# Kernel optimization log

Measured on AMD Instinct MI355X. Metric: run time of the kernel, lower is better.

Reference implementation:

```python
import jax, jax.numpy as jnp
import numpy as np

N = 50000      # num nodes
E = 300000     # num edges
C = 256        # channels
H = 8          # num_heads
DH = C // H    # head_dim = 32
NUM_DST = 256  # dst indices live in [0, NUM_DST) -> anchor columns of BFS frontier
MAX_SPD = 3
EPS = 1e-5     # LayerNorm eps (torch default)


def setup_inputs() -> dict:
    key = jax.random.key(0)
    ks = jax.random.split(key, 10)
    scale = 1.0 / np.sqrt(C).astype(np.float32)
    x = jax.random.normal(ks[0], (N, C), jnp.float32)
    src = jax.random.randint(ks[1], (E,), 0, N, dtype=jnp.int32)
    dst = jax.random.randint(ks[2], (E,), 0, NUM_DST, dtype=jnp.int32)
    Wq = jax.random.normal(ks[3], (C, C), jnp.float32) * scale
    Wk = jax.random.normal(ks[4], (C, C), jnp.float32) * scale
    Wv = jax.random.normal(ks[5], (C, C), jnp.float32) * scale
    bq = jax.random.normal(ks[6], (C,), jnp.float32) * scale
    bk = jax.random.normal(ks[7], (C,), jnp.float32) * scale
    bv = jax.random.normal(ks[8], (C,), jnp.float32) * scale
    spd_w = jax.random.normal(ks[9], (MAX_SPD + 2, H), jnp.float32)
    gamma = jnp.ones((C,), jnp.float32)
    beta = jnp.zeros((C,), jnp.float32)
    return dict(x=x, src=src, dst=dst, Wq=Wq, bq=bq, Wk=Wk, bk=bk,
                Wv=Wv, bv=bv, spd_w=spd_w, gamma=gamma, beta=beta)


def _spd_buckets(src, dst):
    # Reverse-BFS shortest-path buckets (use_reverse=True, directed):
    # A[row=dst, col=src]; F_k = bin(A @ F_{k-1}); anchors are dst nodes,
    # which all live in [0, NUM_DST) so the anchor->column map is identity.
    row, col = dst, src
    F = (jnp.arange(N)[:, None] == jnp.arange(NUM_DST)[None, :]).astype(jnp.float32)  # [N, M]
    spd = jnp.full((E,), MAX_SPD + 1, jnp.int32)
    unset = jnp.ones((E,), bool)
    for k in range(1, MAX_SPD + 1):
        # (A @ F)[i] = sum over edges with row==i of F[col]
        F = (jax.ops.segment_sum(F[col], row, num_segments=N) > 0).astype(jnp.float32)
        reach = F[src, dst] > 0
        newly = unset & reach
        spd = jnp.where(newly, k, spd)
        unset = unset & ~newly
    return spd


def _segment_softmax(scores, seg, n):
    # numerically stable softmax over edges grouped by destination node
    m = jax.ops.segment_max(scores, seg, num_segments=n)
    ex = jnp.exp(scores - m[seg])
    s = jax.ops.segment_sum(ex, seg, num_segments=n)
    return ex / s[seg]


def reference(x, src, dst, Wq, bq, Wk, bk, Wv, bv, spd_w, gamma, beta):
    Q = (x @ Wq.T + bq).reshape(N, H, DH)
    K = (x @ Wk.T + bk).reshape(N, H, DH)
    V = (x @ Wv.T + bv).reshape(N, H, DH)
    # per-edge dot-product scores [E, H]
    scores = (Q[dst] * K[src]).sum(-1) / np.float32(np.sqrt(DH))
    spd = jax.lax.stop_gradient(_spd_buckets(src, dst))  # torch.no_grad
    scores = scores + spd_w[spd]
    w = _segment_softmax(scores, dst, N)  # [E, H] (dropout is identity in eval)
    msg = (V[src] * w[:, :, None]).reshape(E, C)
    out = jax.ops.segment_sum(msg, dst, num_segments=N)  # scatter-add aggregation
    # total degree (in + out) broadcast over channels
    ones_e = jnp.ones((E,), jnp.float32)
    deg = jax.ops.segment_sum(ones_e, src, num_segments=N) + \
          jax.ops.segment_sum(ones_e, dst, num_segments=N)
    h = out + deg[:, None] + x  # residual
    mu = h.mean(-1, keepdims=True)
    var = ((h - mu) ** 2).mean(-1, keepdims=True)
    return (h - mu) / jnp.sqrt(var + EPS) * gamma + beta
```

## Files before the change

### kernel.cpp

```cpp
#include <hip/hip_runtime.h>
#include <stdint.h>

#define N_NODES 50000
#define E_EDGES 300000
#define C_CH    256
#define H_HEADS 8
#define NB2     64
#define CHUNK2  4688
#define NBIN    4096
#define SRCDIV  3125
#define NWG_GEMM 1568
#define NWG_LN   12436
#define GOFF     2

typedef unsigned short u16;
typedef unsigned int   u32;

typedef __attribute__((ext_vector_type(8))) short  v8s;
typedef __attribute__((ext_vector_type(4))) float  v4f;

__device__ __forceinline__ float bf2f(u16 v) {
    union { u32 u; float f; } x; x.u = ((u32)v) << 16; return x.f;
}
__device__ __forceinline__ u16 f2bf(float f) {
    union { float f; u32 u; } x; x.f = f;
    u32 r = (x.u + 0x7FFFu + ((x.u >> 16) & 1u)) >> 16;
    return (u16)r;
}
__device__ __forceinline__ void unp2(u32 v, float& lo, float& hi) {
    union { u32 u; float f; } x;
    x.u = v << 16; lo = x.f;
    x.u = v & 0xFFFF0000u; hi = x.f;
}
__device__ __forceinline__ void gl_lds16(const u16* g, u16* l) {
    __builtin_amdgcn_global_load_lds(
        (const __attribute__((address_space(1))) void*)g,
        (__attribute__((address_space(3))) void*)l, 16, 0, 0);
}
__device__ __forceinline__ void pack8(const float4 p, const float4 q, u16* dst) {
    u16 tmp[8];
    tmp[0]=f2bf(p.x); tmp[1]=f2bf(p.y); tmp[2]=f2bf(p.z); tmp[3]=f2bf(p.w);
    tmp[4]=f2bf(q.x); tmp[5]=f2bf(q.y); tmp[6]=f2bf(q.z); tmp[7]=f2bf(q.w);
    *(uint4*)dst = *(const uint4*)tmp;
}

__global__ __launch_bounds__(256) void prep_k(
    const float* __restrict__ Wk, const float* __restrict__ Wv,
    const float* __restrict__ Wq, u16* __restrict__ Wb,
    const int* __restrict__ src, const int* __restrict__ dst,
    u32* __restrict__ blockhist, u32* __restrict__ pinmask,
    u32* __restrict__ zero0)
{
    __shared__ u32 hist[NBIN];
    __shared__ u32 mask[256][8];
    int t = threadIdx.x, b = blockIdx.x;
    if (b < 192) {
        int m = (b < 64) ? 0 : (b < 128) ? 1 : 2;
        const float* sp = (m == 0) ? Wk : (m == 1) ? Wv : Wq;
        u16* dp = Wb + m * 65536;
        int i = (b & 63) * 1024 + t * 4;
        float4 v = *(const float4*)(sp + i);
        ushort4 o;
        o.x = f2bf(v.x); o.y = f2bf(v.y); o.z = f2bf(v.z); o.w = f2bf(v.w);
        *(ushort4*)(dp + i) = o;
        return;
    }
    if (b >= 256) {
        int z = b - 256;
        uint4 zv = make_uint4(0, 0, 0, 0);
        *(uint4*)(zero0 + z * 1024 + t * 4) = zv;
        return;
    }
    int hb = b - 192;
#pragma unroll
    for (int j = 0; j < 16; j++) hist[t + j * 256] = 0;
#pragma unroll
    for (int w = 0; w < 8; w++) mask[t][w] = 0;
    __syncthreads();
    int start = hb * CHUNK2;
    int end = start + CHUNK2; if (end > E_EDGES) end = E_EDGES;
    for (int e = start + t; e < end; e += 256) {
        int d = dst[e], s = src[e];
        atomicAdd(&hist[d * 16 + s / SRCDIV], 1u);
        if (s < 256) atomicOr(&mask[d][s >> 5], 1u << (s & 31));
    }
    __syncthreads();
#pragma unroll
    for (int j = 0; j < 16; j++)
        blockhist[hb * NBIN + t + j * 256] = hist[t + j * 256];
#pragma unroll
    for (int w = 0; w < 8; w++)
        pinmask[hb * 2048 + w * 256 + t] = mask[t][w];
}

__global__ __launch_bounds__(256, 4) void gemm3(
    const float* __restrict__ x, const u16* __restrict__ Wb,
    const float* __restrict__ bk, const float* __restrict__ bv,
    const float* __restrict__ bq,
    u16* __restrict__ Kb, u16* __restrict__ Vb, u16* __restrict__ Qb,
    const u32* __restrict__ blockhist, u32* __restrict__ bin_off,
    const u32* __restrict__ pinmask, unsigned char* __restrict__ T,
    const float* __restrict__ gamma, const float* __restrict__ beta,
    float* __restrict__ y)
{
    __shared__ u16 smem[4][128 * 32];
    const int t = threadIdx.x;

    if (blockIdx.x == 0) {
        u32* tots = (u32*)&smem[0][0];
        u32* tsum = tots + NBIN;
        u32 c[16];
#pragma unroll
        for (int j = 0; j < 16; j++) c[j] = 0;
        for (int b2 = 0; b2 < NB2; b2++) {
#pragma unroll
            for (int j = 0; j < 16; j++)
                c[j] += blockhist[b2 * NBIN + j * 256 + t];
        }
#pragma unroll
        for (int j = 0; j < 16; j++) tots[j * 256 + t] = c[j];
        __syncthreads();
        u32 loc[16]; u32 a = 0;
#pragma unroll
        for (int j = 0; j < 16; j++) { loc[j] = tots[t * 16 + j]; a += loc[j]; }
        tsum[t] = a;
        __syncthreads();
        for (int off = 1; off < 256; off <<= 1) {
            u32 add = (t >= off) ? tsum[t - off] : 0u;
            __syncthreads();
            tsum[t] += add;
            __syncthreads();
        }
        u32 base = tsum[t] - a;
#pragma unroll
        for (int j = 0; j < 16; j++) { bin_off[t * 16 + j] = base; base += loc[j]; }
        if (t == 255) bin_off[NBIN] = base;
        return;
    }
    if (blockIdx.x == 1) {
        u32* b32 = (u32*)&smem[0][0];
        u32 (*F1)[8] = (u32(*)[8])(b32);
        u32 (*F2)[8] = (u32(*)[8])(b32 + 2048);
        u32 (*F3)[8] = (u32(*)[8])(b32 + 4096);
        int i = t;
        u32 mm[8];
#pragma unroll
        for (int w = 0; w < 8; w++) mm[w] = 0;
        for (int b2 = 0; b2 < NB2; b2++) {
#pragma unroll
            for (int w = 0; w < 8; w++)
                mm[w] |= pinmask[b2 * 2048 + w * 256 + i];
        }
#pragma unroll
        for (int w = 0; w < 8; w++) { F1[i][w] = mm[w]; F2[i][w] = 0; F3[i][w] = 0; }
        __syncthreads();
        for (int w = 0; w < 8; w++) {
            u32 m = F1[i][w];
            while (m) {
                int b = __ffs(m) - 1; m &= m - 1;
                int s = w * 32 + b;
#pragma unroll
                for (int j = 0; j < 8; j++) F2[i][j] |= F1[s][j];
            }
        }
        __syncthreads();
        for (int w = 0; w < 8; w++) {
            u32 m = F1[i][w];
            while (m) {
                int b = __ffs(m) - 1; m &= m - 1;
                int s = w * 32 + b;
#pragma unroll
                for (int j = 0; j < 8; j++) F3[i][j] |= F2[s][j];
            }
        }
        __syncthreads();
        for (int w = 0; w < 8; w++) {
            u32 f1 = F1[i][w], f2 = F2[i][w], f3 = F3[i][w];
#pragma unroll
            for (int g = 0; g < 8; g++) {
                u32 word = 0;
#pragma unroll
                for (int b = 0; b < 4; b++) {
                    int bit = g * 4 + b;
                    u32 k = ((f1 >> bit) & 1u) ? 1u : ((f2 >> bit) & 1u) ? 2u
                           : ((f3 >> bit) & 1u) ? 3u : 4u;
                    word |= k << (8 * b);
                }
                *(u32*)(T + i * 256 + w * 32 + g * 4) = word;
            }
        }
        return;
    }
    if (blockIdx.x >= GOFF + NWG_GEMM) {
        int n = (blockIdx.x - (GOFF + NWG_GEMM)) * 4 + (t >> 6) + 256;
        int lane = t & 63;
        int ch = lane * 4;
        float4 xv = *(const float4*)(x + (size_t)n * 256 + ch);
        float h0 = xv.x, h1 = xv.y, h2 = xv.z, h3 = xv.w;
        float s = h0 + h1 + h2 + h3;
#pragma unroll
        for (int off = 1; off < 64; off <<= 1) s += __shfl_xor(s, off);
        float mu = s * (1.0f / 256.0f);
        float d0 = h0 - mu, d1 = h1 - mu, d2 = h2 - mu, d3 = h3 - mu;
        float qq = d0 * d0 + d1 * d1 + d2 * d2 + d3 * d3;
#pragma unroll
        for (int off = 1; off < 64; off <<= 1) qq += __shfl_xor(qq, off);
        float rstd = rsqrtf(qq * (1.0f / 256.0f) + 1e-5f);
        float4 gv = *(const float4*)(gamma + ch);
        float4 bv = *(const float4*)(beta + ch);
        float4 o;
        o.x = d0 * rstd * gv.x + bv.x;
        o.y = d1 * rstd * gv.y + bv.y;
        o.z = d2 * rstd * gv.z + bv.z;
        o.w = d3 * rstd * gv.w + bv.w;
        *(float4*)(y + (size_t)n * 256 + ch) = o;
        return;
    }

    int gid = blockIdx.x - GOFF;
    int xcd = gid & 7, pos = gid >> 3;
    int wgid = xcd * (NWG_GEMM >> 3) + pos;
    int mt, mat, nh;
    if (wgid < 1564) { mt = wgid >> 2; int j = wgid & 3; mat = j >> 1; nh = j & 1; }
    else             { int qi = wgid - 1564; mt = qi >> 1; mat = 2; nh = qi & 1; }
    const int m0 = mt * 128;
    const int M = (mat == 2) ? 256 : N_NODES;
    const u16* W = Wb + mat * 65536;
    const float* bias = (mat == 0) ? bk : (mat == 1) ? bv : bq;
    u16* OUT = (mat == 0) ? Kb : (mat == 1) ? Vb : Qb;
    const int n0 = nh * 128;

    const int lane = t & 63, w = t >> 6;
    const int quad = lane >> 4, l15 = lane & 15;
    const int mq = w & 1, nq = w >> 1;

    v4f acc[16];
#pragma unroll
    for (int i = 0; i < 16; i++) acc[i] = (v4f)(0.0f);

    const int lrow = lane >> 2;
    const int cg   = (lane & 3) * 8;
    int rA0 = m0 + w * 32 + lrow; if (rA0 > 49999) rA0 = 49999;
    int rA1 = rA0 + 16;           if (rA1 > 49999) rA1 = 49999;
    const float* gA0 = x + (size_t)rA0 * 256 + cg;
    const float* gA1 = x + (size_t)rA1 * 256 + cg;
    const u16* gB = W + (size_t)(n0 + w * 32 + lrow) * 256 + (lane & 3) * 8;

    u16* ldsA = &smem[0][(w * 32 + lrow) * 32 + (lane & 3) * 8];

    float4 a00, a01, a10, a11;
#define LOADA(kt) do {                                   \
    a00 = *(const float4*)(gA0 + (kt) * 32);             \
    a01 = *(const float4*)(gA0 + (kt) * 32 + 4);         \
    a10 = *(const float4*)(gA1 + (kt) * 32);             \
    a11 = *(const float4*)(gA1 + (kt) * 32 + 4);         \
} while (0)
#define WRITEA(bi) do {                                  \
    pack8(a00, a01, ldsA + (bi) * 4096);                 \
    pack8(a10, a11, ldsA + (bi) * 4096 + 16 * 32);       \
} while (0)
#define STAGEB(bi, koff) do {                                             \
    gl_lds16(gB + (koff),            &smem[2 + (bi)][(w * 32) * 32]);     \
    gl_lds16(gB + 16 * 256 + (koff), &smem[2 + (bi)][(w * 32 + 16) * 32]);\
} while (0)

    LOADA(0);
    STAGEB(0, 0);
    WRITEA(0);
    __syncthreads();
    for (int kt = 0; kt < 8; kt++) {
        const int cur = kt & 1;
        if (kt < 7) { LOADA(kt + 1); STAGEB(cur ^ 1, (kt + 1) * 32); }
        v8s a[4], b[4];
#pragma unroll
        for (int f = 0; f < 4; f++)
            a[f] = *(const v8s*)(&smem[cur][(mq * 64 + f * 16 + l15) * 32 + quad * 8]);
#pragma unroll
        for (int f = 0; f < 4; f++)
            b[f] = *(const v8s*)(&smem[2 + cur][(nq * 64 + f * 16 + l15) * 32 + quad * 8]);
#pragma unroll
        for (int fm = 0; fm < 4; fm++)
#pragma unroll
            for (int fn = 0; fn < 4; fn++)
                acc[fm * 4 + fn] = __builtin_amdgcn_mfma_f32_16x16x32_bf16(
                    a[fm], b[fn], acc[fm * 4 + fn], 0, 0, 0);
        if (kt < 7) WRITEA(cur ^ 1);
        __syncthreads();
    }
#undef LOADA
#undef WRITEA
#undef STAGEB

    u16* S = &smem[0][0];
#pragma unroll
    for (int fn = 0; fn < 4; fn++) {
        int n = nq * 64 + fn * 16 + l15;
        float bi = bias[n0 + n];
#pragma unroll
        for (int fm = 0; fm < 4; fm++) {
#pragma unroll
            for (int r2 = 0; r2 < 4; r2++) {
                int row = mq * 64 + fm * 16 + quad * 4 + r2;
                S[row * 128 + n] = f2bf(acc[fm * 4 + fn][r2] + bi);
            }
        }
    }
    __syncthreads();
#pragma unroll
    for (int i = 0; i < 8; i++) {
        int c = i * 256 + t;
        int row = c >> 4;
        int m = m0 + row;
        if (m < M)
            *(uint4*)(OUT + (size_t)m * 256 + n0 + (c & 15) * 8) =
                *(const uint4*)(S + c * 8);
    }
}

__global__ __launch_bounds__(256) void base_k(
    const u32* __restrict__ blockhist, const u32* __restrict__ bin_off,
    u32* __restrict__ blockbase)
{
    int bin = blockIdx.x * 256 + threadIdx.x;
    u32 h[NB2];
#pragma unroll
    for (int b = 0; b < NB2; b++) h[b] = blockhist[b * NBIN + bin];
    u32 run = bin_off[bin];
#pragma unroll
    for (int b = 0; b < NB2; b++) {
        blockbase[b * NBIN + bin] = run;
        run += h[b];
    }
}

__global__ __launch_bounds__(256) void scatter2_k(
    const int* __restrict__ src, const int* __restrict__ dst,
    const u32* __restrict__ blockbase, u32* __restrict__ ssrc)
{
    __shared__ u32 cur[NBIN];
    int t = threadIdx.x, b = blockIdx.x;
#pragma unroll
    for (int j = 0; j < 16; j++)
        cur[t + j * 256] = blockbase[b * NBIN + t + j * 256];
    __syncthreads();
    int start = b * CHUNK2;
    int end = start + CHUNK2; if (end > E_EDGES) end = E_EDGES;
    for (int e = start + t; e < end; e += 256) {
        int s = src[e];
        int bin = dst[e] * 16 + s / SRCDIV;
        u32 pos = atomicAdd(&cur[bin], 1u);
        ssrc[pos] = (u32)s;
    }
}

__global__ __launch_bounds__(256) void agg_k(
    const u32* __restrict__ ssrc, const u32* __restrict__ bin_off,
    const u16* __restrict__ Qb, const u16* __restrict__ Kb,
    const u16* __restrict__ Vb, const unsigned char* __restrict__ T,
    const float* __restrict__ spd_w, float* __restrict__ out,
    float* __restrict__ denom)
{
    __shared__ float red[4 * 256];
    __shared__ float dred[4 * 8];
    int bid = blockIdx.x;
    int d = bid >> 4;
    int t = threadIdx.x, lane = t & 63, wave = t >> 6;
    int half = lane >> 5, sl = lane & 31;
    int h = sl >> 2;
    u32 start = bin_off[bid], end = bin_off[bid + 1];

    uint4 qv = *(const uint4*)(Qb + (size_t)d * 256 + sl * 8);
    float q0,q1,q2,q3,q4,q5,q6,q7;
    unp2(qv.x,q0,q1); unp2(qv.y,q2,q3); unp2(qv.z,q4,q5); unp2(qv.w,q6,q7);
    float sw4 = spd_w[4 * 8 + h];

    float a0=0.f,a1=0.f,a2=0.f,a3=0.f,a4=0.f,a5=0.f,a6=0.f,a7=0.f,dsum=0.f;

    u32 i = start + (u32)(wave * 2 + half);
    int s_c = 0, s_n = 0;
    uint4 kv_c = make_uint4(0,0,0,0), vv_c = kv_c;
    if (i < end) {
        s_c = (int)ssrc[i];
        kv_c = *(const uint4*)(Kb + (size_t)s_c * 256 + sl * 8);
        vv_c = *(const uint4*)(Vb + (size_t)s_c * 256 + sl * 8);
        if (i + 8 < end) s_n = (int)ssrc[i + 8];
    }
    while (i < end) {
        u32 inx = i + 8;
        uint4 kv_n = kv_c, vv_n = vv_c;
        if (inx < end) {
            kv_n = *(const uint4*)(Kb + (size_t)s_n * 256 + sl * 8);
            vv_n = *(const uint4*)(Vb + (size_t)s_n * 256 + sl * 8);
        }
        int s_nn = (inx + 8 < end) ? (int)ssrc[inx + 8] : 0;
        float k0,k1,k2,k3,k4,k5,k6,k7, v0,v1,v2,v3,v4,v5,v6,v7;
        unp2(kv_c.x,k0,k1); unp2(kv_c.y,k2,k3); unp2(kv_c.z,k4,k5); unp2(kv_c.w,k6,k7);
        unp2(vv_c.x,v0,v1); unp2(vv_c.y,v2,v3); unp2(vv_c.z,v4,v5); unp2(vv_c.w,v6,v7);
        float p = q0*k0+q1*k1+q2*k2+q3*k3+q4*k4+q5*k5+q6*k6+q7*k7;
        p += __shfl_xor(p, 1);
        p += __shfl_xor(p, 2);
        float bias = (s_c < 256) ? spd_w[(int)T[s_c * 256 + d] * 8 + h] : sw4;
        float wgt = __expf(p * 0.17677669529663689f + bias);
        a0 += wgt*v0; a1 += wgt*v1; a2 += wgt*v2; a3 += wgt*v3;
        a4 += wgt*v4; a5 += wgt*v5; a6 += wgt*v6; a7 += wgt*v7;
        if ((sl & 3) == 0) dsum += wgt;
        i = inx; s_c = s_n; s_n = s_nn; kv_c = kv_n; vv_c = vv_n;
    }
    a0 += __shfl_xor(a0,32); a1 += __shfl_xor(a1,32);
    a2 += __shfl_xor(a2,32); a3 += __shfl_xor(a3,32);
    a4 += __shfl_xor(a4,32); a5 += __shfl_xor(a5,32);
    a6 += __shfl_xor(a6,32); a7 += __shfl_xor(a7,32);
    dsum += __shfl_xor(dsum,32);
    if (half == 0) {
        *(float4*)(&red[wave * 256 + sl * 8])     = make_float4(a0,a1,a2,a3);
        *(float4*)(&red[wave * 256 + sl * 8 + 4]) = make_float4(a4,a5,a6,a7);
        if ((sl & 3) == 0) dred[wave * 8 + h] = dsum;
    }
    __syncthreads();
    float sAll = red[t] + red[256 + t] + red[512 + t] + red[768 + t];
    atomicAdd(&out[(size_t)d * 256 + t], sAll);
    if (t < 8) {
        float ds = dred[t] + dred[8 + t] + dred[16 + t] + dred[24 + t];
        atomicAdd(&denom[d * 8 + t], ds);
    }
}

__global__ __launch_bounds__(256) void ln_k(
    const float* __restrict__ x, const float* __restrict__ out,
    const float* __restrict__ denom, const float* __restrict__ gamma,
    const float* __restrict__ beta, float* __restrict__ y)
{
    int n = blockIdx.x * 4 + (threadIdx.x >> 6);
    int lane = threadIdx.x & 63;
    int ch = lane * 4;
    float4 xv = *(const float4*)(x + (size_t)n * 256 + ch);
    float h0 = xv.x, h1 = xv.y, h2 = xv.z, h3 = xv.w;
    float den = denom[n * 8 + (lane >> 3)];
    float inv = (den > 0.f) ? 1.0f / den : 0.0f;
    const float* op = out + (size_t)n * 256 + ch;
    h0 += op[0] * inv; h1 += op[1] * inv;
    h2 += op[2] * inv; h3 += op[3] * inv;
    float s = h0 + h1 + h2 + h3;
#pragma unroll
    for (int off = 1; off < 64; off <<= 1) s += __shfl_xor(s, off);
    float mu = s * (1.0f / 256.0f);
    float d0 = h0 - mu, d1 = h1 - mu, d2 = h2 - mu, d3 = h3 - mu;
    float q = d0 * d0 + d1 * d1 + d2 * d2 + d3 * d3;
#pragma unroll
    for (int off = 1; off < 64; off <<= 1) q += __shfl_xor(q, off);
    float rstd = rsqrtf(q * (1.0f / 256.0f) + 1e-5f);
    float4 gv = *(const float4*)(gamma + ch);
    float4 bv = *(const float4*)(beta + ch);
    float4 o;
    o.x = d0 * rstd * gv.x + bv.x;
    o.y = d1 * rstd * gv.y + bv.y;
    o.z = d2 * rstd * gv.z + bv.z;
    o.w = d3 * rstd * gv.w + bv.w;
    *(float4*)(y + (size_t)n * 256 + ch) = o;
}

extern "C" void kernel_launch(void* const* d_in, const int* in_sizes, int n_in,
                              void* d_out, int out_size, void* d_ws, size_t ws_size,
                              hipStream_t stream)
{
    const float* x     = (const float*)d_in[0];
    const int*   src   = (const int*)d_in[1];
    const int*   dst   = (const int*)d_in[2];
    const float* Wq    = (const float*)d_in[3];
    const float* bq    = (const float*)d_in[4];
    const float* Wk    = (const float*)d_in[5];
    const float* bk    = (const float*)d_in[6];
    const float* Wv    = (const float*)d_in[7];
    const float* bv    = (const float*)d_in[8];
    const float* spd_w = (const float*)d_in[9];
    const float* gamma = (const float*)d_in[10];
    const float* beta  = (const float*)d_in[11];
    float* y = (float*)d_out;

    char* ws = (char*)d_ws;
    float* denom     = (float*)(ws + 0);
    float* outf      = (float*)(ws + 8192);
    u32*   bin_off   = (u32*)(ws + 270336);
    unsigned char* T = (unsigned char*)(ws + 286976);
    u32*   blockhist = (u32*)(ws + 352512);
    u32*   pinmask   = (u32*)(ws + 1401088);
    u32*   blockbase = (u32*)(ws + 1925376);
    u32*   ssrc      = (u32*)(ws + 2973952);
    u16*   Qb        = (u16*)(ws + 4202752);
    u16*   Kb        = (u16*)(ws + 4333824);
    u16*   Vb        = (u16*)(ws + 29933824);
    u16*   Wb        = (u16*)(ws + 55533824);

    dim3 blk(256);
    prep_k<<<dim3(322), blk, 0, stream>>>(Wk, Wv, Wq, Wb, src, dst,
                                          blockhist, pinmask, (u32*)(ws + 0));
    gemm3<<<dim3(GOFF + NWG_GEMM + NWG_LN), blk, 0, stream>>>(
        x, Wb, bk, bv, bq, Kb, Vb, Qb, blockhist, bin_off, pinmask, T,
        gamma, beta, y);
    base_k<<<dim3(16), blk, 0, stream>>>(blockhist, bin_off, blockbase);
    scatter2_k<<<dim3(NB2), blk, 0, stream>>>(src, dst, blockbase, ssrc);
    agg_k<<<dim3(NBIN), blk, 0, stream>>>(ssrc, bin_off, Qb, Kb, Vb, T, spd_w, outf, denom);
    ln_k<<<dim3(64), blk, 0, stream>>>(x, outf, denom, gamma, beta, y);
}
```

Before: 200.7 us.

## Fold bin-base computation and edge scatter into gemm3 side blocks

Removes the separate base_k and scatter2_k launches. 64 extra blocks are added at the front of gemm3. Each recomputes the global bin prefix sum plus its own per-chunk prefix from blockhist, then scatters its edge chunk into ssrc. The aim is to cut two kernel launches and the blockbase buffer, and to overlap the sort scatter with the projection GEMM. In exchange, every scatter block redundantly reads the whole histogram and runs a 256-wide scan, and the GEMM grid gets longer.

```diff
diff --git a/kernel.cpp b/kernel.cpp
--- a/kernel.cpp
+++ b/kernel.cpp
@@ -11,7 +11,7 @@
 #define SRCDIV  3125
 #define NWG_GEMM 1568
 #define NWG_LN   12436
-#define GOFF     2
+#define GOFF     66
 
 typedef unsigned short u16;
 typedef unsigned int   u32;
@@ -100,15 +100,17 @@
     u16* __restrict__ Kb, u16* __restrict__ Vb, u16* __restrict__ Qb,
     const u32* __restrict__ blockhist, u32* __restrict__ bin_off,
     const u32* __restrict__ pinmask, unsigned char* __restrict__ T,
+    const int* __restrict__ src, const int* __restrict__ dst,
+    u32* __restrict__ ssrc,
     const float* __restrict__ gamma, const float* __restrict__ beta,
     float* __restrict__ y)
 {
     __shared__ u16 smem[4][128 * 32];
+    __shared__ u32 ts[256];
     const int t = threadIdx.x;
 
     if (blockIdx.x == 0) {
         u32* tots = (u32*)&smem[0][0];
-        u32* tsum = tots + NBIN;
         u32 c[16];
 #pragma unroll
         for (int j = 0; j < 16; j++) c[j] = 0;
@@ -123,15 +125,15 @@
         u32 loc[16]; u32 a = 0;
 #pragma unroll
         for (int j = 0; j < 16; j++) { loc[j] = tots[t * 16 + j]; a += loc[j]; }
-        tsum[t] = a;
+        ts[t] = a;
         __syncthreads();
         for (int off = 1; off < 256; off <<= 1) {
-            u32 add = (t >= off) ? tsum[t - off] : 0u;
+            u32 add = (t >= off) ? ts[t - off] : 0u;
             __syncthreads();
-            tsum[t] += add;
+            ts[t] += add;
             __syncthreads();
         }
-        u32 base = tsum[t] - a;
+        u32 base = ts[t] - a;
 #pragma unroll
         for (int j = 0; j < 16; j++) { bin_off[t * 16 + j] = base; base += loc[j]; }
         if (t == 255) bin_off[NBIN] = base;
@@ -188,6 +190,60 @@
                 }
                 *(u32*)(T + i * 256 + w * 32 + g * 4) = word;
             }
+        }
+        return;
+    }
+    if (blockIdx.x < GOFF) {
+        int b = blockIdx.x - 2;
+        u32* tots = (u32*)&smem[0][0];
+        u32* pre  = tots + NBIN;
+        u32 ctot[16], cpre[16];
+#pragma unroll
+        for (int j = 0; j < 16; j++) { ctot[j] = 0; cpre[j] = 0; }
+        for (int b2 = 0; b2 < NB2; b2++) {
+#pragma unroll
+            for (int j = 0; j < 16; j++) {
+                u32 h = blockhist[b2 * NBIN + j * 256 + t];
+                ctot[j] += h;
+                if (b2 < b) cpre[j] += h;
+            }
+        }
+#pragma unroll
+        for (int j = 0; j < 16; j++) {
+            tots[j * 256 + t] = ctot[j];
+            pre[j * 256 + t]  = cpre[j];
+        }
+        __syncthreads();
+        u32 loc[16], prer[16]; u32 a = 0;
+#pragma unroll
+        for (int j = 0; j < 16; j++) {
+            loc[j] = tots[t * 16 + j];
+            prer[j] = pre[t * 16 + j];
+            a += loc[j];
+        }
+        ts[t] = a;
+        __syncthreads();
+        for (int off = 1; off < 256; off <<= 1) {
+            u32 add = (t >= off) ? ts[t - off] : 0u;
+            __syncthreads();
+            ts[t] += add;
+            __syncthreads();
+        }
+        u32 run = ts[t] - a;
+        u32* cur = tots;
+#pragma unroll
+        for (int j = 0; j < 16; j++) {
+            cur[t * 16 + j] = run + prer[j];
+            run += loc[j];
+        }
+        __syncthreads();
+        int start = b * CHUNK2;
+        int end = start + CHUNK2; if (end > E_EDGES) end = E_EDGES;
+        for (int e = start + t; e < end; e += 256) {
+            int s = src[e];
+            int bin = dst[e] * 16 + s / SRCDIV;
+            u32 pos = atomicAdd(&cur[bin], 1u);
+            ssrc[pos] = (u32)s;
         }
         return;
     }
@@ -314,42 +370,6 @@
         if (m < M)
             *(uint4*)(OUT + (size_t)m * 256 + n0 + (c & 15) * 8) =
                 *(const uint4*)(S + c * 8);
-    }
-}
-
-__global__ __launch_bounds__(256) void base_k(
-    const u32* __restrict__ blockhist, const u32* __restrict__ bin_off,
-    u32* __restrict__ blockbase)
-{
-    int bin = blockIdx.x * 256 + threadIdx.x;
-    u32 h[NB2];
-#pragma unroll
-    for (int b = 0; b < NB2; b++) h[b] = blockhist[b * NBIN + bin];
-    u32 run = bin_off[bin];
-#pragma unroll
-    for (int b = 0; b < NB2; b++) {
-        blockbase[b * NBIN + bin] = run;
-        run += h[b];
-    }
-}
-
-__global__ __launch_bounds__(256) void scatter2_k(
-    const int* __restrict__ src, const int* __restrict__ dst,
-    const u32* __restrict__ blockbase, u32* __restrict__ ssrc)
-{
-    __shared__ u32 cur[NBIN];
-    int t = threadIdx.x, b = blockIdx.x;
-#pragma unroll
-    for (int j = 0; j < 16; j++)
-        cur[t + j * 256] = blockbase[b * NBIN + t + j * 256];
-    __syncthreads();
-    int start = b * CHUNK2;
-    int end = start + CHUNK2; if (end > E_EDGES) end = E_EDGES;
-    for (int e = start + t; e < end; e += 256) {
-        int s = src[e];
-        int bin = dst[e] * 16 + s / SRCDIV;
-        u32 pos = atomicAdd(&cur[bin], 1u);
-        ssrc[pos] = (u32)s;
     }
 }
 
@@ -484,21 +504,18 @@
     unsigned char* T = (unsigned char*)(ws + 286976);
     u32*   blockhist = (u32*)(ws + 352512);
     u32*   pinmask   = (u32*)(ws + 1401088);
-    u32*   blockbase = (u32*)(ws + 1925376);
-    u32*   ssrc      = (u32*)(ws + 2973952);
-    u16*   Qb        = (u16*)(ws + 4202752);
-    u16*   Kb        = (u16*)(ws + 4333824);
-    u16*   Vb        = (u16*)(ws + 29933824);
-    u16*   Wb        = (u16*)(ws + 55533824);
+    u32*   ssrc      = (u32*)(ws + 1925376);
+    u16*   Qb        = (u16*)(ws + 3125376);
+    u16*   Kb        = (u16*)(ws + 3256448);
+    u16*   Vb        = (u16*)(ws + 28881024);
+    u16*   Wb        = (u16*)(ws + 54505600);
 
     dim3 blk(256);
     prep_k<<<dim3(322), blk, 0, stream>>>(Wk, Wv, Wq, Wb, src, dst,
                                           blockhist, pinmask, (u32*)(ws + 0));
     gemm3<<<dim3(GOFF + NWG_GEMM + NWG_LN), blk, 0, stream>>>(
         x, Wb, bk, bv, bq, Kb, Vb, Qb, blockhist, bin_off, pinmask, T,
-        gamma, beta, y);
-    base_k<<<dim3(16), blk, 0, stream>>>(blockhist, bin_off, blockbase);
-    scatter2_k<<<dim3(NB2), blk, 0, stream>>>(src, dst, blockbase, ssrc);
+        src, dst, ssrc, gamma, beta, y);
     agg_k<<<dim3(NBIN), blk, 0, stream>>>(ssrc, bin_off, Qb, Kb, Vb, T, spd_w, outf, denom);
     ln_k<<<dim3(64), blk, 0, stream>>>(x, outf, denom, gamma, beta, y);
 }
```

New measurement: 197.2 us. About the same (-1.8%).
